# Performance work log

Measured on AMD Instinct MI355X. Metric: run time of the kernel, lower is better.

## Reference

```python
import jax, jax.numpy as jnp
import numpy as np

N = 100000        # unique nodes in batch (node_num)
IN_DIM = 256
OUT_DIM = 128
E_RAND = 1_600_000  # random graph edges (avg degree 16)
B = N             # batch nodes (all nodes, each gets a self-loop edge)
SLOPE = 0.1       # leaky_relu slope_ratio


def setup_inputs() -> dict:
    key = jax.random.key(0)
    k1, k2, k3, k4, k5, k6 = jax.random.split(key, 6)
    x = jax.random.normal(k1, (N, IN_DIM), dtype=jnp.float32)
    # small weight scale keeps exp(leaky_relu(.)) in a sane range, like kaiming on unit-ish inputs
    W = jax.random.normal(k2, (OUT_DIM, IN_DIM), dtype=jnp.float32) * 0.05
    b = jax.random.normal(k3, (OUT_DIM,), dtype=jnp.float32) * 0.05
    a = jax.random.normal(k4, (2 * OUT_DIM, 1), dtype=jnp.float32) * 0.05
    src = jax.random.randint(k5, (E_RAND,), 0, N, dtype=jnp.int32)
    dst = jax.random.randint(k6, (E_RAND,), 0, N, dtype=jnp.int32)
    batch_idx = jnp.arange(B, dtype=jnp.int32)
    # append self-loop edges for every batch node (original vstacks original_node_edge)
    edges = jnp.stack([jnp.concatenate([src, batch_idx]),
                       jnp.concatenate([dst, batch_idx])], axis=1)  # [E_TOT, 2]
    return {"x": x, "W": W, "b": b, "a": a, "edges": edges, "batch_idx": batch_idx}


def reference(x, W, b, a, edges, batch_idx):
    # new_embeddings = Linear(in_dim -> out_dim)
    emb = x @ W.T + b  # [N, out_dim]
    # concat(h_src, h_dst) @ a  ==  h_src @ a[:d] + h_dst @ a[d:]
    a1 = a[:OUT_DIM, 0]
    a2 = a[OUT_DIM:, 0]
    s_src = emb @ a1  # [N]
    s_dst = emb @ a2  # [N]
    src, dst = edges[:, 0], edges[:, 1]
    logits = s_src[src] + s_dst[dst]                                 # [E]
    score = jnp.exp(jax.nn.leaky_relu(logits, negative_slope=SLOPE))  # [E]
    # sparse row-sum and aggregation fused as segment reductions over src
    row_sum = jax.ops.segment_sum(score, src, num_segments=N)        # [N]
    msgs = score[:, None] * emb[dst]                                 # [E, out_dim]
    results = jax.ops.segment_sum(msgs, src, num_segments=N)         # [N, out_dim]
    # nodes with no outgoing edges have row_sum==0; they are never gathered below
    safe_rs = jnp.where(row_sum > 0, row_sum, 1.0)
    out = results / safe_rs[:, None]
    return out[batch_idx]
```

## Files before the change

kernel.cpp:

```cpp
#include <hip/hip_runtime.h>
#include <hip/hip_fp16.h>

#define IN_DIM 256
#define OUT_DIM 128
#define SLOPE 0.1f
#define EPB 4096
#define BSH 8

typedef __attribute__((ext_vector_type(8))) short short8;
typedef __attribute__((ext_vector_type(4))) float f32x4;

__device__ __forceinline__ unsigned bf16_rne(float f) {
    unsigned u = __float_as_uint(f);
    return (u + 0x7FFFu + ((u >> 16) & 1u)) >> 16;
}

__global__ __launch_bounds__(256) void wsplit_pass0_kernel(
    const float* __restrict__ W, short* __restrict__ Whi, short* __restrict__ Wlo,
    const int* __restrict__ edges, int* __restrict__ bucket_cnt, int E, int K)
{
    __shared__ int hist[4096];
    const int tid = threadIdx.x;
    if ((int)blockIdx.x < 128) {
        const int i = blockIdx.x * 256 + tid;
        const float v = W[i];
        const unsigned hb = bf16_rne(v);
        const float hf = __uint_as_float(hb << 16);
        Whi[i] = (short)hb;
        Wlo[i] = (short)bf16_rne(v - hf);
        return;
    }
    const int pb = (int)blockIdx.x - 128;
    for (int t = tid; t < K; t += 256) hist[t] = 0;
    __syncthreads();
    const int e0 = pb * EPB;
    #pragma unroll
    for (int i = 0; i < EPB / 256; ++i) {
        const int e = e0 + i * 256 + tid;
        if (e < E) {
            const int src = ((const int2*)edges)[e].x;
            atomicAdd(&hist[src >> BSH], 1);
        }
    }
    __syncthreads();
    for (int t = tid; t < K; t += 256)
        if (hist[t]) atomicAdd(&bucket_cnt[t], hist[t]);
}

__global__ __launch_bounds__(256) void scan_ident_kernel(
    const int* __restrict__ bucket_cnt, int* __restrict__ bucket_base,
    int* __restrict__ gcursor, int* __restrict__ off,
    const int* __restrict__ bidx, int* __restrict__ flag, int N, int E, int K)
{
    const int tid = threadIdx.x;
    if (blockIdx.x == 0) {
        __shared__ int sc[4098];
        for (int t = tid; t < K; t += 256) sc[t] = bucket_cnt[t];
        __syncthreads();
        if (tid == 0) {
            int run = 0;
            for (int b = 0; b < K; ++b) { const int c = sc[b]; sc[b] = run; run += c; }
            sc[K] = run;
        }
        __syncthreads();
        for (int t = tid; t <= K; t += 256) {
            bucket_base[t] = sc[t];
            if (t < K) gcursor[t] = sc[t];
        }
        if (tid == 0) off[N] = E;
    }
    const int i = blockIdx.x * 256 + tid;
    if (i < N && bidx[i] != i) atomicOr(flag, 1);
}

__global__ __launch_bounds__(256) void gemm_pass1_kernel(
    const float* __restrict__ x, const short* __restrict__ Whi_g,
    const short* __restrict__ Wlo_g, const float* __restrict__ bias,
    const float* __restrict__ a, __half* __restrict__ emb_h,
    float* __restrict__ s1, float* __restrict__ s2,
    const int* __restrict__ edges, int* __restrict__ gcursor,
    int2* __restrict__ tmp, int N, int E, int K, int nP1)
{
    __shared__ short lds[12288];

    const int tid = threadIdx.x;

    if ((int)blockIdx.x < nP1) {
        int* hist  = (int*)lds;
        int* baseL = hist + K;
        int* curL  = baseL + K;
        for (int t = tid; t < K; t += 256) { hist[t] = 0; curL[t] = 0; }
        __syncthreads();
        const int e0 = (int)blockIdx.x * EPB;
        #pragma unroll
        for (int i = 0; i < EPB / 256; ++i) {
            const int e = e0 + i * 256 + tid;
            if (e < E) {
                const int src = ((const int2*)edges)[e].x;
                atomicAdd(&hist[src >> BSH], 1);
            }
        }
        __syncthreads();
        for (int t = tid; t < K; t += 256)
            if (hist[t]) baseL[t] = atomicAdd(&gcursor[t], hist[t]);
        __syncthreads();
        #pragma unroll
        for (int i = 0; i < EPB / 256; ++i) {
            const int e = e0 + i * 256 + tid;
            if (e < E) {
                const int2 ed = ((const int2*)edges)[e];
                const int b = ed.x >> BSH;
                const int s = atomicAdd(&curL[b], 1);
                tmp[baseL[b] + s] = ed;
            }
        }
        return;
    }

    short* Ahi = lds;
    short* Alo = lds + 2048;
    short* Bhi = lds + 4096;
    short* Blo = lds + 8192;

    const int l   = tid & 63;
    const int w   = tid >> 6;
    const int gm0 = ((int)blockIdx.x - nP1) * 64;

    const int arow = tid >> 2;
    const int akc  = tid & 3;
    const int gmA  = gm0 + arow;
    const bool av_ok = (gmA < N);
    const int brow = tid >> 1;
    const int bkc0 = (tid & 1) * 2;

    short8 xh[8], xl[8];
    #pragma unroll
    for (int ks = 0; ks < 8; ++ks) {
        float v[8];
        if (av_ok) {
            const float4 p0 = *(const float4*)&x[(size_t)gmA * IN_DIM + ks * 32 + akc * 8];
            const float4 p1 = *(const float4*)&x[(size_t)gmA * IN_DIM + ks * 32 + akc * 8 + 4];
            v[0]=p0.x; v[1]=p0.y; v[2]=p0.z; v[3]=p0.w;
            v[4]=p1.x; v[5]=p1.y; v[6]=p1.z; v[7]=p1.w;
        } else {
            #pragma unroll
            for (int j = 0; j < 8; ++j) v[j] = 0.f;
        }
        short8 h8, l8;
        #pragma unroll
        for (int j = 0; j < 8; ++j) {
            unsigned hb = bf16_rne(v[j]);
            float hf = __uint_as_float(hb << 16);
            h8[j] = (short)hb;
            l8[j] = (short)bf16_rne(v[j] - hf);
        }
        xh[ks] = h8;
        xl[ks] = l8;
    }
    const int awoff = akc * 512 + ((arow ^ akc) * 8);

    f32x4 acc[8];
    #pragma unroll
    for (int j = 0; j < 8; ++j) acc[j] = (f32x4)0.f;

    float bias_v[8], av1[8], av2[8];
    #pragma unroll
    for (int nf = 0; nf < 8; ++nf) {
        const int col = nf * 16 + (l & 15);
        bias_v[nf] = bias[col];
        av1[nf]    = a[col];
        av2[nf]    = a[OUT_DIM + col];
    }

    #pragma unroll
    for (int ks = 0; ks < 8; ++ks) {
        const int k0 = ks * 32;
        *(short8*)&Ahi[awoff] = xh[ks];
        *(short8*)&Alo[awoff] = xl[ks];
        #pragma unroll
        for (int q = 0; q < 2; ++q) {
            const int kc = bkc0 + q;
            const short8 h8 = *(const short8*)&Whi_g[brow * IN_DIM + k0 + kc * 8];
            const short8 l8 = *(const short8*)&Wlo_g[brow * IN_DIM + k0 + kc * 8];
            *(short8*)&Bhi[kc * 1024 + brow * 8] = h8;
            *(short8*)&Blo[kc * 1024 + brow * 8] = l8;
        }
        __syncthreads();

        const int kcr    = l >> 4;
        const int arow_f = w * 16 + (l & 15);
        const int aoff   = kcr * 512 + ((arow_f ^ kcr) * 8);
        const short8 ah = *(const short8*)&Ahi[aoff];
        const short8 al = *(const short8*)&Alo[aoff];
        #pragma unroll
        for (int nf = 0; nf < 8; ++nf) {
            const int col = nf * 16 + (l & 15);
            const int boff = kcr * 1024 + col * 8;
            const short8 bh = *(const short8*)&Bhi[boff];
            const short8 bl = *(const short8*)&Blo[boff];
            acc[nf] = __builtin_amdgcn_mfma_f32_16x16x32_bf16(ah, bh, acc[nf], 0, 0, 0);
            acc[nf] = __builtin_amdgcn_mfma_f32_16x16x32_bf16(al, bh, acc[nf], 0, 0, 0);
            acc[nf] = __builtin_amdgcn_mfma_f32_16x16x32_bf16(ah, bl, acc[nf], 0, 0, 0);
        }
        __syncthreads();
    }

    __half* hl = (__half*)lds;
    #pragma unroll
    for (int r = 0; r < 4; ++r) {
        const int lrow = w * 16 + (l >> 4) * 4 + r;
        float p1 = 0.f, p2 = 0.f;
        #pragma unroll
        for (int nf = 0; nf < 8; ++nf) {
            const float e = acc[nf][r] + bias_v[nf];
            p1 += e * av1[nf];
            p2 += e * av2[nf];
            hl[lrow * 144 + nf * 16 + (l & 15)] = __float2half(e);
        }
        p1 += __shfl_xor(p1, 1); p1 += __shfl_xor(p1, 2);
        p1 += __shfl_xor(p1, 4); p1 += __shfl_xor(p1, 8);
        p2 += __shfl_xor(p2, 1); p2 += __shfl_xor(p2, 2);
        p2 += __shfl_xor(p2, 4); p2 += __shfl_xor(p2, 8);
        const int gm = gm0 + lrow;
        if ((l & 15) == 0 && gm < N) { s1[gm] = p1; s2[gm] = p2; }
    }
    __syncthreads();
    #pragma unroll
    for (int i = 0; i < 4; ++i) {
        const int idx = i * 256 + tid;
        const int row = idx >> 4, seg = idx & 15;
        if (gm0 + row < N) {
            const uint4 u = *(const uint4*)&hl[row * 144 + seg * 8];
            ((uint4*)emb_h)[(size_t)(gm0 + row) * 16 + seg] = u;
        }
    }
}

__global__ __launch_bounds__(256) void pass2_kernel(
    const int2* __restrict__ tmp, const int* __restrict__ bucket_base,
    int* __restrict__ off, int* __restrict__ csr, int N)
{
    __shared__ int cnt[256];
    __shared__ int cur[256];

    const int tid = threadIdx.x;
    const int b   = blockIdx.x;
    const int v0  = b << BSH;
    const int nloc = min(256, N - v0);
    const int s0 = bucket_base[b];
    const int cntE = bucket_base[b + 1] - s0;

    cnt[tid] = 0;
    __syncthreads();
    for (int e = tid; e < cntE; e += 256)
        atomicAdd(&cnt[tmp[s0 + e].x - v0], 1);
    __syncthreads();

    const int ts = cnt[tid];
    cur[tid] = ts;
    __syncthreads();
    for (int d = 1; d < 256; d <<= 1) {
        int xv = (tid >= d) ? cur[tid - d] : 0;
        __syncthreads();
        cur[tid] += xv;
        __syncthreads();
    }
    const int mypre = cur[tid] - ts;
    __syncthreads();
    cur[tid] = mypre;
    if (tid < nloc) off[v0 + tid] = s0 + mypre;
    __syncthreads();

    for (int e = tid; e < cntE; e += 256) {
        const int2 ed = tmp[s0 + e];
        const int sl = atomicAdd(&cur[ed.x - v0], 1);
        csr[s0 + sl] = ed.y;
    }
}

__global__ __launch_bounds__(256) void agg_kernel(
    const int* __restrict__ off, const int* __restrict__ csr,
    const float* __restrict__ s1, const float* __restrict__ s2,
    const __half* __restrict__ emb_h, const int* __restrict__ flag,
    float* __restrict__ results, float* __restrict__ out, int N)
{
    __shared__ int2 sl[4][64];

    const int wid  = (int)((blockIdx.x * 256u + threadIdx.x) >> 6);
    const int lane = threadIdx.x & 63;
    const int wv   = threadIdx.x >> 6;
    if (wid >= N) return;
    const int eg = lane >> 4;
    const int cl = lane & 15;
    const int beg = off[wid];
    const int end = off[wid + 1];
    const float s1n = s1[wid];

    const float4* __restrict__ embrow = (const float4*)emb_h;
    int2* slot = &sl[wv][0];

    float av[8];
    #pragma unroll
    for (int k = 0; k < 8; ++k) av[k] = 0.f;
    float rsl = 0.f;

    for (int tile = beg; tile < end; tile += 64) {
        const int cnt = min(64, end - tile);
        int d = 0; float sc = 0.f;
        if (lane < cnt) {
            d = csr[tile + lane];
            const float ll = s1n + s2[d];
            sc = __expf(ll > 0.f ? ll : SLOPE * ll);
        }
        rsl += sc;
        slot[lane] = make_int2(d, __float_as_int(sc));
        __builtin_amdgcn_wave_barrier();
        for (int j0 = 0; j0 < cnt; j0 += 32) {
            const int nq = ((cnt - j0) + 3) >> 2;
            int dq[8]; float scq[8];
            #pragma unroll
            for (int q = 0; q < 8; ++q) {
                dq[q] = 0; scq[q] = 0.f;
                if (q < nq) {
                    const int2 p = slot[j0 + q * 4 + eg];
                    dq[q] = p.x; scq[q] = __int_as_float(p.y);
                }
            }
            float4 vq[8];
            #pragma unroll
            for (int q = 0; q < 8; ++q)
                if (q < nq) vq[q] = embrow[(size_t)dq[q] * 16 + cl];
            #pragma unroll
            for (int q = 0; q < 8; ++q) {
                if (q < nq) {
                    const unsigned* up = reinterpret_cast<const unsigned*>(&vq[q]);
                    #pragma unroll
                    for (int p = 0; p < 4; ++p) {
                        asm("v_fma_mix_f32 %0, %1, %2, %0 op_sel:[0,0,0] op_sel_hi:[1,0,0]"
                            : "+v"(av[2 * p]) : "v"(up[p]), "v"(scq[q]));
                        asm("v_fma_mix_f32 %0, %1, %2, %0 op_sel:[1,0,0] op_sel_hi:[1,0,0]"
                            : "+v"(av[2 * p + 1]) : "v"(up[p]), "v"(scq[q]));
                    }
                }
            }
        }
        __builtin_amdgcn_wave_barrier();
    }

    float rs = rsl;
    rs += __shfl_xor(rs, 1);  rs += __shfl_xor(rs, 2);
    rs += __shfl_xor(rs, 4);  rs += __shfl_xor(rs, 8);
    rs += __shfl_xor(rs, 16); rs += __shfl_xor(rs, 32);
    #pragma unroll
    for (int k = 0; k < 8; ++k) {
        av[k] += __shfl_xor(av[k], 16);
        av[k] += __shfl_xor(av[k], 32);
    }

    const float inv = 1.f / (rs > 0.f ? rs : 1.f);
    if (eg == 0) {
        float* dbuf = (*flag == 0) ? out : results;
        float4* rp = (float4*)&dbuf[(size_t)wid * 128 + cl * 8];
        rp[0] = make_float4(av[0] * inv, av[1] * inv, av[2] * inv, av[3] * inv);
        rp[1] = make_float4(av[4] * inv, av[5] * inv, av[6] * inv, av[7] * inv);
    }
}

__global__ __launch_bounds__(256) void gather_kernel(
    const float* __restrict__ results, const int* __restrict__ bidx,
    const int* __restrict__ flag, float* __restrict__ out, int N)
{
    if (*flag == 0) return;
    const unsigned i = blockIdx.x * 256u + threadIdx.x;
    if (i >= (unsigned)N * 32u) return;
    const unsigned n = i >> 5, c = i & 31;
    ((float4*)out)[i] = ((const float4*)results)[(size_t)bidx[n] * 32 + c];
}

extern "C" void kernel_launch(void* const* d_in, const int* in_sizes, int n_in,
                              void* d_out, int out_size, void* d_ws, size_t ws_size,
                              hipStream_t stream) {
    const float* x     = (const float*)d_in[0];
    const float* W     = (const float*)d_in[1];
    const float* b     = (const float*)d_in[2];
    const float* a     = (const float*)d_in[3];
    const int*   edges = (const int*)d_in[4];
    const int*   bidx  = (const int*)d_in[5];

    const int N = in_sizes[5];
    const int E = in_sizes[4] / 2;
    const int K = (N + 255) >> BSH;

    float*  results = (float*)d_ws;
    __half* emb_h   = (__half*)(results + (size_t)N * OUT_DIM);
    int2*   tmp     = (int2*)(emb_h + (size_t)N * OUT_DIM);
    int*    csr     = (int*)(tmp + E);
    float*  s1      = (float*)(csr + E);
    float*  s2      = s1 + N;
    int*    off     = (int*)(s2 + N);
    int*    bucket_cnt  = off + N + 1;
    int*    flag        = bucket_cnt + K;
    int*    bucket_base = flag + 1;
    int*    gcursor     = bucket_base + K + 1;
    short*  Whi     = (short*)(gcursor + K);
    short*  Wlo     = Whi + OUT_DIM * IN_DIM;

    hipMemsetAsync(bucket_cnt, 0, (size_t)(K + 1) * sizeof(int), stream);

    const int nP = (E + EPB - 1) / EPB;

    wsplit_pass0_kernel<<<128 + nP, 256, 0, stream>>>(
        W, Whi, Wlo, edges, bucket_cnt, E, K);

    const int nIdent = (N + 255) / 256;
    scan_ident_kernel<<<nIdent, 256, 0, stream>>>(
        bucket_cnt, bucket_base, gcursor, off, bidx, flag, N, E, K);

    const int nGemm = (N + 63) / 64;
    gemm_pass1_kernel<<<nP + nGemm, 256, 0, stream>>>(
        x, Whi, Wlo, b, a, emb_h, s1, s2, edges, gcursor, tmp, N, E, K, nP);

    pass2_kernel<<<K, 256, 0, stream>>>(tmp, bucket_base, off, csr, N);

    const unsigned aggThreads = (unsigned)N * 64u;
    agg_kernel<<<(aggThreads + 255u) / 256u, 256, 0, stream>>>(
        off, csr, s1, s2, emb_h, flag, results, (float*)d_out, N);

    const unsigned gatherThreads = (unsigned)N * 32u;
    gather_kernel<<<(gatherThreads + 255u) / 256u, 256, 0, stream>>>(
        results, bidx, flag, (float*)d_out, N);
}
```

Baseline: 185.4 us.

## Precompute edge scores in CSR build and stream (dst,score) pairs into aggregation

Moves the per-edge score computation (s1+s2 gather, leaky-relu, exp) from the aggregation kernel into pass2, which now writes interleaved (dst, score) int2 records in CSR order. The aggregation kernel then reads these pairs directly per lane group, drops the LDS staging, the wave barriers and the per-tile scoring step, and uses a full 32-edge unrolled main loop plus a tail. This doubles CSR write and read traffic, and pass2 now does random s1/s2 gathers, in exchange for a shorter critical path in the gather-heavy aggregation.

```diff
diff --git a/kernel.cpp b/kernel.cpp
--- a/kernel.cpp
+++ b/kernel.cpp
@@ -238,7 +238,8 @@
 
 __global__ __launch_bounds__(256) void pass2_kernel(
     const int2* __restrict__ tmp, const int* __restrict__ bucket_base,
-    int* __restrict__ off, int* __restrict__ csr, int N)
+    const float* __restrict__ s1, const float* __restrict__ s2,
+    int* __restrict__ off, int2* __restrict__ edata, int N)
 {
     __shared__ int cnt[256];
     __shared__ int cur[256];
@@ -273,89 +274,96 @@
 
     for (int e = tid; e < cntE; e += 256) {
         const int2 ed = tmp[s0 + e];
+        const float ll = s1[ed.x] + s2[ed.y];
+        const float sc = __expf(ll > 0.f ? ll : SLOPE * ll);
         const int sl = atomicAdd(&cur[ed.x - v0], 1);
-        csr[s0 + sl] = ed.y;
+        edata[s0 + sl] = make_int2(ed.y, __float_as_int(sc));
     }
 }
 
 __global__ __launch_bounds__(256) void agg_kernel(
-    const int* __restrict__ off, const int* __restrict__ csr,
-    const float* __restrict__ s1, const float* __restrict__ s2,
+    const int* __restrict__ off, const int2* __restrict__ edata,
     const __half* __restrict__ emb_h, const int* __restrict__ flag,
     float* __restrict__ results, float* __restrict__ out, int N)
 {
-    __shared__ int2 sl[4][64];
-
     const int wid  = (int)((blockIdx.x * 256u + threadIdx.x) >> 6);
     const int lane = threadIdx.x & 63;
-    const int wv   = threadIdx.x >> 6;
     if (wid >= N) return;
     const int eg = lane >> 4;
     const int cl = lane & 15;
     const int beg = off[wid];
     const int end = off[wid + 1];
-    const float s1n = s1[wid];
 
     const float4* __restrict__ embrow = (const float4*)emb_h;
-    int2* slot = &sl[wv][0];
 
     float av[8];
     #pragma unroll
     for (int k = 0; k < 8; ++k) av[k] = 0.f;
-    float rsl = 0.f;
-
-    for (int tile = beg; tile < end; tile += 64) {
-        const int cnt = min(64, end - tile);
-        int d = 0; float sc = 0.f;
-        if (lane < cnt) {
-            d = csr[tile + lane];
-            const float ll = s1n + s2[d];
-            sc = __expf(ll > 0.f ? ll : SLOPE * ll);
-        }
-        rsl += sc;
-        slot[lane] = make_int2(d, __float_as_int(sc));
-        __builtin_amdgcn_wave_barrier();
-        for (int j0 = 0; j0 < cnt; j0 += 32) {
-            const int nq = ((cnt - j0) + 3) >> 2;
-            int dq[8]; float scq[8];
+    float rs = 0.f;
+
+    int base = beg;
+    for (; base + 32 <= end; base += 32) {
+        int2 pq[8];
+        #pragma unroll
+        for (int q = 0; q < 8; ++q)
+            pq[q] = edata[base + q * 4 + eg];
+        float4 vq[8];
+        #pragma unroll
+        for (int q = 0; q < 8; ++q)
+            vq[q] = embrow[(size_t)pq[q].x * 16 + cl];
+        #pragma unroll
+        for (int q = 0; q < 8; ++q) {
+            const float sc = __int_as_float(pq[q].y);
+            rs += sc;
+            const unsigned* up = reinterpret_cast<const unsigned*>(&vq[q]);
             #pragma unroll
-            for (int q = 0; q < 8; ++q) {
-                dq[q] = 0; scq[q] = 0.f;
-                if (q < nq) {
-                    const int2 p = slot[j0 + q * 4 + eg];
-                    dq[q] = p.x; scq[q] = __int_as_float(p.y);
+            for (int p = 0; p < 4; ++p) {
+                asm("v_fma_mix_f32 %0, %1, %2, %0 op_sel:[0,0,0] op_sel_hi:[1,0,0]"
+                    : "+v"(av[2 * p]) : "v"(up[p]), "v"(sc));
+                asm("v_fma_mix_f32 %0, %1, %2, %0 op_sel:[1,0,0] op_sel_hi:[1,0,0]"
+                    : "+v"(av[2 * p + 1]) : "v"(up[p]), "v"(sc));
+            }
+        }
+    }
+    if (base < end) {
+        const int nq = ((end - base) + 3) >> 2;
+        int2 pq[8];
+        #pragma unroll
+        for (int q = 0; q < 8; ++q) {
+            pq[q] = make_int2(0, 0);
+            if (q < nq) {
+                const int idx = base + q * 4 + eg;
+                if (idx < end) pq[q] = edata[idx];
+            }
+        }
+        float4 vq[8];
+        #pragma unroll
+        for (int q = 0; q < 8; ++q)
+            if (q < nq) vq[q] = embrow[(size_t)pq[q].x * 16 + cl];
+        #pragma unroll
+        for (int q = 0; q < 8; ++q) {
+            if (q < nq) {
+                const float sc = __int_as_float(pq[q].y);
+                rs += sc;
+                const unsigned* up = reinterpret_cast<const unsigned*>(&vq[q]);
+                #pragma unroll
+                for (int p = 0; p < 4; ++p) {
+                    asm("v_fma_mix_f32 %0, %1, %2, %0 op_sel:[0,0,0] op_sel_hi:[1,0,0]"
+                        : "+v"(av[2 * p]) : "v"(up[p]), "v"(sc));
+                    asm("v_fma_mix_f32 %0, %1, %2, %0 op_sel:[1,0,0] op_sel_hi:[1,0,0]"
+                        : "+v"(av[2 * p + 1]) : "v"(up[p]), "v"(sc));
                 }
             }
-            float4 vq[8];
-            #pragma unroll
-            for (int q = 0; q < 8; ++q)
-                if (q < nq) vq[q] = embrow[(size_t)dq[q] * 16 + cl];
-            #pragma unroll
-            for (int q = 0; q < 8; ++q) {
-                if (q < nq) {
-                    const unsigned* up = reinterpret_cast<const unsigned*>(&vq[q]);
-                    #pragma unroll
-                    for (int p = 0; p < 4; ++p) {
-                        asm("v_fma_mix_f32 %0, %1, %2, %0 op_sel:[0,0,0] op_sel_hi:[1,0,0]"
-                            : "+v"(av[2 * p]) : "v"(up[p]), "v"(scq[q]));
-                        asm("v_fma_mix_f32 %0, %1, %2, %0 op_sel:[1,0,0] op_sel_hi:[1,0,0]"
-                            : "+v"(av[2 * p + 1]) : "v"(up[p]), "v"(scq[q]));
-                    }
-                }
-            }
-        }
-        __builtin_amdgcn_wave_barrier();
-    }
-
-    float rs = rsl;
-    rs += __shfl_xor(rs, 1);  rs += __shfl_xor(rs, 2);
-    rs += __shfl_xor(rs, 4);  rs += __shfl_xor(rs, 8);
-    rs += __shfl_xor(rs, 16); rs += __shfl_xor(rs, 32);
+        }
+    }
+
     #pragma unroll
     for (int k = 0; k < 8; ++k) {
         av[k] += __shfl_xor(av[k], 16);
         av[k] += __shfl_xor(av[k], 32);
     }
+    rs += __shfl_xor(rs, 16);
+    rs += __shfl_xor(rs, 32);
 
     const float inv = 1.f / (rs > 0.f ? rs : 1.f);
     if (eg == 0) {
@@ -394,8 +402,8 @@
     float*  results = (float*)d_ws;
     __half* emb_h   = (__half*)(results + (size_t)N * OUT_DIM);
     int2*   tmp     = (int2*)(emb_h + (size_t)N * OUT_DIM);
-    int*    csr     = (int*)(tmp + E);
-    float*  s1      = (float*)(csr + E);
+    int2*   edata   = tmp + E;
+    float*  s1      = (float*)(edata + E);
     float*  s2      = s1 + N;
     int*    off     = (int*)(s2 + N);
     int*    bucket_cnt  = off + N + 1;
@@ -420,11 +428,11 @@
     gemm_pass1_kernel<<<nP + nGemm, 256, 0, stream>>>(
         x, Whi, Wlo, b, a, emb_h, s1, s2, edges, gcursor, tmp, N, E, K, nP);
 
-    pass2_kernel<<<K, 256, 0, stream>>>(tmp, bucket_base, off, csr, N);
+    pass2_kernel<<<K, 256, 0, stream>>>(tmp, bucket_base, s1, s2, off, edata, N);
 
     const unsigned aggThreads = (unsigned)N * 64u;
     agg_kernel<<<(aggThreads + 255u) / 256u, 256, 0, stream>>>(
-        off, csr, s1, s2, emb_h, flag, results, (float*)d_out, N);
+        off, edata, emb_h, flag, results, (float*)d_out, N);
 
     const unsigned gatherThreads = (unsigned)N * 32u;
     gather_kernel<<<(gatherThreads + 255u) / 256u, 256, 0, stream>>>(
```

After: 194.3 us. 1.05x slower.
